# Optimization experiments

Measured on AMD Instinct MI355X. Metric: run time of the kernel, lower is better.

Reference implementation:

```python
import jax, jax.numpy as jnp
import numpy as np

N = 4096
IN_F = 256
OUT_F = 64
K = 4
ALPHA = 0.2  # LeakyReLU negative slope
NEG_INF = -9e15


def setup_inputs() -> dict:
    key = jax.random.key(0)
    k_h, k_w, k_a, k_e, k_m = jax.random.split(key, 5)
    h = jax.random.normal(k_h, (N, IN_F), dtype=jnp.float32)
    # xavier_uniform with gain=1.414
    def xavier(k, shape, gain=1.414):
        fan_in, fan_out = shape[0], shape[1]
        limit = gain * np.sqrt(6.0 / (fan_in + fan_out))
        return jax.random.uniform(k, shape, jnp.float32, -limit, limit)
    W = xavier(k_w, (IN_F, OUT_F))
    a = xavier(k_a, (2 * OUT_F, 1))
    vals = jax.random.uniform(k_e, (K, N, N), dtype=jnp.float32)
    mask = jax.random.uniform(k_m, (K, N, N), dtype=jnp.float32) < 0.05
    edge_attr = jnp.where(mask, vals, 0.0)
    return {"h": h, "edge_attr": edge_attr, "W": W, "a": a}


def reference(h, edge_attr, W, a):
    # h: [N, IN_F], edge_attr: [K, N, N], W: [IN_F, OUT_F], a: [2*OUT_F, 1]
    Wh = h @ W                                   # [N, OUT_F]
    Wh1 = Wh @ a[:OUT_F, :]                      # [N, 1]
    Wh2 = Wh @ a[OUT_F:, :]                      # [N, 1]
    e = jax.nn.leaky_relu(Wh1 + Wh2.T, negative_slope=ALPHA)  # [N, N]
    e = e[None, :, :] * edge_attr                # [K, N, N]
    e = jnp.where(edge_attr > 0, e, NEG_INF)
    att = jax.nn.softmax(e, axis=1)              # softmax over dim=1, as in torch
    # dropout is identity in eval mode
    # batched replacement for the per-channel python loop of matmuls
    hp = jnp.einsum('kij,jf->kif', att, Wh)      # [K, N, OUT_F]
    out = jnp.transpose(hp, (1, 0, 2)).reshape(N, K * OUT_F)  # concat dim=1
    return jax.nn.elu(out), att
```

## Files before the change

### kernel.cpp

```cpp
#include <hip/hip_runtime.h>

#define NN 4096
#define IN_F 256
#define OUT_F 64
#define K_CH 4
#define ALPHA 0.2f
#define ROWS1 32
#define IC1 128
#define BSTRIDE 264

typedef __bf16 bf16;
typedef __attribute__((ext_vector_type(8))) __bf16 bf16x8;
typedef __attribute__((ext_vector_type(4))) __bf16 bf16x4;
typedef __attribute__((ext_vector_type(4))) float f32x4;

__global__ __launch_bounds__(256) void k0_wh(const float* __restrict__ h,
                                             const float* __restrict__ W,
                                             const float* __restrict__ a,
                                             float* __restrict__ Wh,
                                             float* __restrict__ Wh1,
                                             float* __restrict__ Wh2) {
    int tid = threadIdx.x;
    int wave = tid >> 6, lane = tid & 63;
    int i = blockIdx.x * 4 + wave;
    const float* hrow = h + (size_t)i * IN_F;
    float acc = 0.f;
    #pragma unroll 8
    for (int c = 0; c < IN_F; ++c)
        acc += hrow[c] * W[c * OUT_F + lane];
    Wh[(size_t)i * OUT_F + lane] = acc;
    float v1 = acc * a[lane];
    float v2 = acc * a[OUT_F + lane];
    #pragma unroll
    for (int o = 32; o > 0; o >>= 1) {
        v1 += __shfl_xor(v1, o, 64);
        v2 += __shfl_xor(v2, o, 64);
    }
    if (lane == 0) { Wh1[i] = v1; Wh2[i] = v2; }
}

__global__ __launch_bounds__(256) void k0_transpose(const float* __restrict__ Wh,
                                                    bf16* __restrict__ WhT) {
    __shared__ float lds[OUT_F * 65];
    int tid = threadIdx.x;
    int i0 = blockIdx.x * 64;
    int f = tid & 63;
    int r0 = tid >> 6;
    #pragma unroll
    for (int s = 0; s < 16; ++s) {
        int r = r0 * 16 + s;
        lds[f * 65 + r] = Wh[(size_t)(i0 + r) * OUT_F + f];
    }
    __syncthreads();
    int f2 = tid >> 2;
    int c0 = (tid & 3) * 16;
    bf16x8 v0, v1;
    #pragma unroll
    for (int s = 0; s < 8; ++s) {
        v0[s] = (bf16)lds[f2 * 65 + c0 + s];
        v1[s] = (bf16)lds[f2 * 65 + c0 + 8 + s];
    }
    *(bf16x8*)&WhT[(size_t)f2 * NN + i0 + c0] = v0;
    *(bf16x8*)&WhT[(size_t)f2 * NN + i0 + c0 + 8] = v1;
}

__global__ __launch_bounds__(256) void k1_colsum(const float* __restrict__ edge,
                                                 const float* __restrict__ Wh1,
                                                 const float* __restrict__ Wh2,
                                                 bf16* __restrict__ p_buf,
                                                 float* __restrict__ partial) {
    int tid = threadIdx.x;
    int kch = blockIdx.z;
    int j0 = blockIdx.y * 1024 + tid * 4;
    int ic = blockIdx.x;
    int ibase = ic * ROWS1;
    f32x4 w2 = *(const f32x4*)&Wh2[j0];
    f32x4 w1v[ROWS1 / 4];
    #pragma unroll
    for (int t = 0; t < ROWS1 / 4; ++t)
        w1v[t] = *(const f32x4*)&Wh1[ibase + t * 4];
    f32x4 s = {0.f, 0.f, 0.f, 0.f};
    const float* base = edge + ((size_t)kch * NN + ibase) * NN + j0;
    bf16* pbase = p_buf + ((size_t)kch * NN + ibase) * NN + j0;
    f32x4 r[8];
    #pragma unroll
    for (int t = 0; t < 8; ++t)
        r[t] = __builtin_nontemporal_load((const f32x4*)(base + (size_t)t * NN));
    #pragma unroll
    for (int ii = 0; ii < ROWS1; ++ii) {
        int cur = ii & 7;
        f32x4 e = r[cur];
        int ip = (ii + 8 < ROWS1) ? ii + 8 : ii;
        r[cur] = __builtin_nontemporal_load((const f32x4*)(base + (size_t)ip * NN));
        float wh1 = w1v[ii >> 2][ii & 3];
        bf16x4 pv;
        #pragma unroll
        for (int c = 0; c < 4; ++c) {
            float xv = wh1 + w2[c];
            float lk = xv > 0.f ? xv : ALPHA * xv;
            float val = e[c] > 0.f ? __expf(lk * e[c]) : 0.f;
            bf16 vb = (bf16)val;
            pv[c] = vb;
            s[c] += (float)vb;
        }
        *(bf16x4*)(pbase + (size_t)ii * NN) = pv;
    }
    *(f32x4*)(partial + ((size_t)kch * IC1 + ic) * NN + j0) = s;
}

__global__ __launch_bounds__(256) void k1_reduce(const float* __restrict__ partial,
                                                 const bf16* __restrict__ WhT,
                                                 float* __restrict__ s_inv,
                                                 bf16* __restrict__ WhTs) {
    __shared__ float red[256];
    __shared__ float inv_l[64];
    int tid = threadIdx.x;
    int kch = blockIdx.y;
    int jl = tid & 63, g = tid >> 6;
    int jbase = blockIdx.x * 64;
    int j = jbase + jl;
    const float* pb = partial + (size_t)kch * IC1 * NN;
    float s = 0.f;
    #pragma unroll 8
    for (int t = 0; t < IC1 / 4; ++t)
        s += pb[(size_t)(g * (IC1 / 4) + t) * NN + j];
    red[tid] = s;
    __syncthreads();
    if (tid < 64) {
        float tot = red[tid] + red[tid + 64] + red[tid + 128] + red[tid + 192];
        float iv = tot > 0.f ? 1.f / tot : 0.f;
        s_inv[kch * NN + j] = iv;
        inv_l[tid] = iv;
    }
    __syncthreads();
    int f = tid >> 2;
    int c0 = (tid & 3) * 16;
    bf16x8 a0 = *(const bf16x8*)&WhT[(size_t)f * NN + jbase + c0];
    bf16x8 a1 = *(const bf16x8*)&WhT[(size_t)f * NN + jbase + c0 + 8];
    bf16x8 o0, o1;
    #pragma unroll
    for (int s2 = 0; s2 < 8; ++s2) {
        o0[s2] = (bf16)((float)a0[s2] * inv_l[c0 + s2]);
        o1[s2] = (bf16)((float)a1[s2] * inv_l[c0 + 8 + s2]);
    }
    bf16* wb = WhTs + ((size_t)kch * OUT_F + f) * NN + jbase + c0;
    *(bf16x8*)wb = o0;
    *(bf16x8*)(wb + 8) = o1;
}

__global__ __launch_bounds__(256) void k2_mfma(const bf16* __restrict__ p_buf,
                                               const bf16* __restrict__ WhTs,
                                               float* __restrict__ out) {
    __shared__ bf16 ldsB[OUT_F * BSTRIDE];
    int tid = threadIdx.x;
    int itile = blockIdx.x;
    int kch = blockIdx.y;
    int wave = tid >> 6, lane = tid & 63;
    int n16 = lane & 15, quad = lane >> 4;
    int i_row = itile * 64 + wave * 16 + n16;
    const bf16* pptr = p_buf + ((size_t)kch * NN + i_row) * NN + quad * 8;
    f32x4 acc[4] = {};
    bf16x8 pf[8];
    #pragma unroll
    for (int t = 0; t < 8; ++t)
        pf[t] = __builtin_nontemporal_load((const bf16x8*)(pptr + t * 32));
    int f = tid >> 2, part = (tid & 3) * 64;
    const bf16* wsrc = WhTs + ((size_t)kch * OUT_F + f) * NN + part;
    for (int slab = 0; slab < 16; ++slab) {
        __syncthreads();
        #pragma unroll
        for (int u = 0; u < 8; ++u) {
            bf16x8 v = *(const bf16x8*)(wsrc + slab * 256 + u * 8);
            *(bf16x8*)&ldsB[f * BSTRIDE + part + u * 8] = v;
        }
        __syncthreads();
        #pragma unroll
        for (int t = 0; t < 8; ++t) {
            int g = slab * 8 + t;
            int cur = g & 7;
            bf16x8 afrag = pf[cur];
            int gp = (g + 8 < 128) ? g + 8 : g;
            pf[cur] = __builtin_nontemporal_load((const bf16x8*)(pptr + gp * 32));
            int jl = t * 32 + quad * 8;
            #pragma unroll
            for (int ft = 0; ft < 4; ++ft) {
                bf16x8 bfrag = *(const bf16x8*)&ldsB[(ft * 16 + n16) * BSTRIDE + jl];
                acc[ft] = __builtin_amdgcn_mfma_f32_16x16x32_bf16(afrag, bfrag, acc[ft], 0, 0, 0);
            }
        }
    }
    #pragma unroll
    for (int ft = 0; ft < 4; ++ft) {
        #pragma unroll
        for (int r = 0; r < 4; ++r) {
            int row_l = quad * 4 + r;
            int i_g = itile * 64 + wave * 16 + row_l;
            float v = acc[ft][r];
            out[(size_t)i_g * (K_CH * OUT_F) + kch * OUT_F + ft * 16 + n16] =
                v > 0.f ? v : __expf(v) - 1.f;
        }
    }
}

__global__ __launch_bounds__(256) void k2_att(const bf16* __restrict__ p_buf,
                                              const float* __restrict__ s_inv,
                                              float* __restrict__ att_out) {
    int kch = blockIdx.y;
    const bf16* pb = p_buf + (size_t)kch * NN * NN;
    float* ab = att_out + (size_t)kch * NN * NN;
    const float* inv = s_inv + kch * NN;
    #pragma unroll
    for (int it = 0; it < 4; ++it) {
        size_t chunk = ((size_t)it * 2048 + blockIdx.x) * 256 + threadIdx.x;
        size_t base = chunk * 8;
        int j0 = (int)(base & (NN - 1));
        bf16x8 pv = __builtin_nontemporal_load((const bf16x8*)(pb + base));
        f32x4 iv0 = *(const f32x4*)&inv[j0];
        f32x4 iv1 = *(const f32x4*)&inv[j0 + 4];
        f32x4 a0, a1;
        #pragma unroll
        for (int c = 0; c < 4; ++c) {
            a0[c] = (float)pv[c] * iv0[c];
            a1[c] = (float)pv[c + 4] * iv1[c];
        }
        __builtin_nontemporal_store(a0, (f32x4*)(ab + base));
        __builtin_nontemporal_store(a1, (f32x4*)(ab + base + 4));
    }
}

extern "C" void kernel_launch(void* const* d_in, const int* in_sizes, int n_in,
                              void* d_out, int out_size, void* d_ws, size_t ws_size,
                              hipStream_t stream) {
    (void)out_size; (void)ws_size;
    const float *h = nullptr, *edge = nullptr, *W = nullptr, *a = nullptr;
    for (int i = 0; i < n_in; ++i) {
        int sz = in_sizes[i];
        if (sz == NN * IN_F)               h    = (const float*)d_in[i];
        else if (sz == K_CH * NN * NN)     edge = (const float*)d_in[i];
        else if (sz == IN_F * OUT_F)       W    = (const float*)d_in[i];
        else if (sz == 2 * OUT_F)          a    = (const float*)d_in[i];
    }

    char* ws = (char*)d_ws;
    size_t off = 0;
    float* Wh      = (float*)(ws + off); off += (size_t)NN * OUT_F * 4;
    float* Wh1     = (float*)(ws + off); off += NN * 4;
    float* Wh2     = (float*)(ws + off); off += NN * 4;
    float* s_inv   = (float*)(ws + off); off += (size_t)K_CH * NN * 4;
    bf16*  WhT     = (bf16*) (ws + off); off += (size_t)OUT_F * NN * 2;
    bf16*  WhTs    = (bf16*) (ws + off); off += (size_t)K_CH * OUT_F * NN * 2;
    float* partial = (float*)(ws + off); off += (size_t)K_CH * IC1 * NN * 4;
    bf16*  p_buf   = (bf16*) (ws + off); off += (size_t)K_CH * NN * NN * 2;

    float* out_h   = (float*)d_out;
    float* att_out = out_h + (size_t)NN * (K_CH * OUT_F);

    k0_wh<<<dim3(NN / 4), 256, 0, stream>>>(h, W, a, Wh, Wh1, Wh2);
    k0_transpose<<<dim3(NN / 64), 256, 0, stream>>>(Wh, WhT);
    k1_colsum<<<dim3(IC1, 4, K_CH), 256, 0, stream>>>(edge, Wh1, Wh2, p_buf, partial);
    k1_reduce<<<dim3(NN / 64, K_CH), 256, 0, stream>>>(partial, WhT, s_inv, WhTs);
    k2_mfma<<<dim3(64, K_CH), 256, 0, stream>>>(p_buf, WhTs, out_h);
    k2_att<<<dim3(2048, K_CH), 256, 0, stream>>>(p_buf, s_inv, att_out);
}
```

Before: 565.2 us.

## Recompute attention weights from edge data instead of materializing bf16 buffer

Drops the bf16 p_buf intermediate. The column-sum kernel now only produces partial sums. A fused kernel re-reads edge_attr, recomputes the exponentials, writes the normalized attention, and feeds the MFMA aggregation in one pass. The j dimension is split into four chunks for more blocks, with a small ELU reduction kernel summing the partial outputs. This removes a write and two reads of the large bf16 buffer in exchange for a second read of the fp32 edge tensor and extra exp work.

```diff
diff --git a/kernel.cpp b/kernel.cpp
--- a/kernel.cpp
+++ b/kernel.cpp
@@ -67,7 +67,6 @@
 __global__ __launch_bounds__(256) void k1_colsum(const float* __restrict__ edge,
                                                  const float* __restrict__ Wh1,
                                                  const float* __restrict__ Wh2,
-                                                 bf16* __restrict__ p_buf,
                                                  float* __restrict__ partial) {
     int tid = threadIdx.x;
     int kch = blockIdx.z;
@@ -81,29 +80,24 @@
         w1v[t] = *(const f32x4*)&Wh1[ibase + t * 4];
     f32x4 s = {0.f, 0.f, 0.f, 0.f};
     const float* base = edge + ((size_t)kch * NN + ibase) * NN + j0;
-    bf16* pbase = p_buf + ((size_t)kch * NN + ibase) * NN + j0;
     f32x4 r[8];
     #pragma unroll
     for (int t = 0; t < 8; ++t)
-        r[t] = __builtin_nontemporal_load((const f32x4*)(base + (size_t)t * NN));
+        r[t] = *(const f32x4*)(base + (size_t)t * NN);
     #pragma unroll
     for (int ii = 0; ii < ROWS1; ++ii) {
-        int cur = ii & 7;
-        f32x4 e = r[cur];
-        int ip = (ii + 8 < ROWS1) ? ii + 8 : ii;
-        r[cur] = __builtin_nontemporal_load((const f32x4*)(base + (size_t)ip * NN));
+        f32x4 e = r[ii & 7];
+        if (ii + 8 < ROWS1)
+            r[ii & 7] = *(const f32x4*)(base + (size_t)(ii + 8) * NN);
         float wh1 = w1v[ii >> 2][ii & 3];
-        bf16x4 pv;
         #pragma unroll
         for (int c = 0; c < 4; ++c) {
             float xv = wh1 + w2[c];
             float lk = xv > 0.f ? xv : ALPHA * xv;
             float val = e[c] > 0.f ? __expf(lk * e[c]) : 0.f;
             bf16 vb = (bf16)val;
-            pv[c] = vb;
             s[c] += (float)vb;
         }
-        *(bf16x4*)(pbase + (size_t)ii * NN) = pv;
     }
     *(f32x4*)(partial + ((size_t)kch * IC1 + ic) * NN + j0) = s;
 }
@@ -148,25 +142,38 @@
     *(bf16x8*)(wb + 8) = o1;
 }
 
-__global__ __launch_bounds__(256) void k2_mfma(const bf16* __restrict__ p_buf,
-                                               const bf16* __restrict__ WhTs,
-                                               float* __restrict__ out) {
+__global__ __launch_bounds__(256, 4) void k2_fused(const float* __restrict__ edge,
+                                                   const float* __restrict__ Wh1,
+                                                   const float* __restrict__ Wh2,
+                                                   const float* __restrict__ s_inv,
+                                                   const bf16* __restrict__ WhTs,
+                                                   float* __restrict__ att_out,
+                                                   float* __restrict__ hp_part) {
     __shared__ bf16 ldsB[OUT_F * BSTRIDE];
     int tid = threadIdx.x;
     int itile = blockIdx.x;
-    int kch = blockIdx.y;
+    int jq = blockIdx.y;
+    int kch = blockIdx.z;
     int wave = tid >> 6, lane = tid & 63;
     int n16 = lane & 15, quad = lane >> 4;
     int i_row = itile * 64 + wave * 16 + n16;
-    const bf16* pptr = p_buf + ((size_t)kch * NN + i_row) * NN + quad * 8;
+    int jbase = jq * 1024;
+    const float* erow = edge + ((size_t)kch * NN + i_row) * NN + jbase + quad * 8;
+    float* arow = att_out + ((size_t)kch * NN + i_row) * NN + jbase + quad * 8;
+    const float* w2p = Wh2 + jbase + quad * 8;
+    const float* ivp = s_inv + kch * NN + jbase + quad * 8;
+    float wh1 = Wh1[i_row];
     f32x4 acc[4] = {};
-    bf16x8 pf[8];
-    #pragma unroll
-    for (int t = 0; t < 8; ++t)
-        pf[t] = __builtin_nontemporal_load((const bf16x8*)(pptr + t * 32));
+    f32x4 pf0[4], pf1[4];
+    #pragma unroll
+    for (int t = 0; t < 4; ++t) {
+        pf0[t] = *(const f32x4*)(erow + t * 32);
+        pf1[t] = *(const f32x4*)(erow + t * 32 + 4);
+    }
     int f = tid >> 2, part = (tid & 3) * 64;
-    const bf16* wsrc = WhTs + ((size_t)kch * OUT_F + f) * NN + part;
-    for (int slab = 0; slab < 16; ++slab) {
+    const bf16* wsrc = WhTs + ((size_t)kch * OUT_F + f) * NN + jbase + part;
+    #pragma unroll
+    for (int slab = 0; slab < 4; ++slab) {
         __syncthreads();
         #pragma unroll
         for (int u = 0; u < 8; ++u) {
@@ -177,10 +184,33 @@
         #pragma unroll
         for (int t = 0; t < 8; ++t) {
             int g = slab * 8 + t;
-            int cur = g & 7;
-            bf16x8 afrag = pf[cur];
-            int gp = (g + 8 < 128) ? g + 8 : g;
-            pf[cur] = __builtin_nontemporal_load((const bf16x8*)(pptr + gp * 32));
+            int cur = g & 3;
+            f32x4 e0 = pf0[cur], e1 = pf1[cur];
+            if (g + 4 < 32) {
+                pf0[cur] = *(const f32x4*)(erow + (g + 4) * 32);
+                pf1[cur] = *(const f32x4*)(erow + (g + 4) * 32 + 4);
+            }
+            f32x4 w2a = *(const f32x4*)(w2p + g * 32);
+            f32x4 w2b = *(const f32x4*)(w2p + g * 32 + 4);
+            f32x4 iva = *(const f32x4*)(ivp + g * 32);
+            f32x4 ivb = *(const f32x4*)(ivp + g * 32 + 4);
+            bf16x8 afrag;
+            f32x4 av0, av1;
+            #pragma unroll
+            for (int c = 0; c < 8; ++c) {
+                float e  = c < 4 ? e0[c]  : e1[c - 4];
+                float wv = c < 4 ? w2a[c] : w2b[c - 4];
+                float iv = c < 4 ? iva[c] : ivb[c - 4];
+                float xv = wh1 + wv;
+                float lk = xv > 0.f ? xv : ALPHA * xv;
+                float val = e > 0.f ? __expf(lk * e) : 0.f;
+                bf16 vb = (bf16)val;
+                afrag[c] = vb;
+                float attv = (float)vb * iv;
+                if (c < 4) av0[c] = attv; else av1[c - 4] = attv;
+            }
+            *(f32x4*)(arow + g * 32) = av0;
+            *(f32x4*)(arow + g * 32 + 4) = av1;
             int jl = t * 32 + quad * 8;
             #pragma unroll
             for (int ft = 0; ft < 4; ++ft) {
@@ -189,43 +219,27 @@
             }
         }
     }
+    float* hb = hp_part + (((size_t)kch * 4 + jq) * NN) * OUT_F;
     #pragma unroll
     for (int ft = 0; ft < 4; ++ft) {
         #pragma unroll
         for (int r = 0; r < 4; ++r) {
-            int row_l = quad * 4 + r;
-            int i_g = itile * 64 + wave * 16 + row_l;
-            float v = acc[ft][r];
-            out[(size_t)i_g * (K_CH * OUT_F) + kch * OUT_F + ft * 16 + n16] =
-                v > 0.f ? v : __expf(v) - 1.f;
-        }
-    }
-}
-
-__global__ __launch_bounds__(256) void k2_att(const bf16* __restrict__ p_buf,
-                                              const float* __restrict__ s_inv,
-                                              float* __restrict__ att_out) {
-    int kch = blockIdx.y;
-    const bf16* pb = p_buf + (size_t)kch * NN * NN;
-    float* ab = att_out + (size_t)kch * NN * NN;
-    const float* inv = s_inv + kch * NN;
-    #pragma unroll
-    for (int it = 0; it < 4; ++it) {
-        size_t chunk = ((size_t)it * 2048 + blockIdx.x) * 256 + threadIdx.x;
-        size_t base = chunk * 8;
-        int j0 = (int)(base & (NN - 1));
-        bf16x8 pv = __builtin_nontemporal_load((const bf16x8*)(pb + base));
-        f32x4 iv0 = *(const f32x4*)&inv[j0];
-        f32x4 iv1 = *(const f32x4*)&inv[j0 + 4];
-        f32x4 a0, a1;
-        #pragma unroll
-        for (int c = 0; c < 4; ++c) {
-            a0[c] = (float)pv[c] * iv0[c];
-            a1[c] = (float)pv[c + 4] * iv1[c];
-        }
-        __builtin_nontemporal_store(a0, (f32x4*)(ab + base));
-        __builtin_nontemporal_store(a1, (f32x4*)(ab + base + 4));
-    }
+            int i_g = itile * 64 + wave * 16 + quad * 4 + r;
+            hb[(size_t)i_g * OUT_F + ft * 16 + n16] = acc[ft][r];
+        }
+    }
+}
+
+__global__ __launch_bounds__(256) void k3_elu(const float* __restrict__ hp_part,
+                                              float* __restrict__ out) {
+    int i = blockIdx.x;
+    int tid = threadIdx.x;
+    int kch = tid >> 6, f = tid & 63;
+    float s = 0.f;
+    #pragma unroll
+    for (int jq = 0; jq < 4; ++jq)
+        s += hp_part[(((size_t)kch * 4 + jq) * NN + i) * OUT_F + f];
+    out[(size_t)i * (K_CH * OUT_F) + tid] = s > 0.f ? s : __expf(s) - 1.f;
 }
 
 extern "C" void kernel_launch(void* const* d_in, const int* in_sizes, int n_in,
@@ -250,15 +264,16 @@
     bf16*  WhT     = (bf16*) (ws + off); off += (size_t)OUT_F * NN * 2;
     bf16*  WhTs    = (bf16*) (ws + off); off += (size_t)K_CH * OUT_F * NN * 2;
     float* partial = (float*)(ws + off); off += (size_t)K_CH * IC1 * NN * 4;
-    bf16*  p_buf   = (bf16*) (ws + off); off += (size_t)K_CH * NN * NN * 2;
+    float* hp_part = (float*)(ws + off); off += (size_t)K_CH * 4 * NN * OUT_F * 4;
 
     float* out_h   = (float*)d_out;
     float* att_out = out_h + (size_t)NN * (K_CH * OUT_F);
 
     k0_wh<<<dim3(NN / 4), 256, 0, stream>>>(h, W, a, Wh, Wh1, Wh2);
     k0_transpose<<<dim3(NN / 64), 256, 0, stream>>>(Wh, WhT);
-    k1_colsum<<<dim3(IC1, 4, K_CH), 256, 0, stream>>>(edge, Wh1, Wh2, p_buf, partial);
+    k1_colsum<<<dim3(IC1, 4, K_CH), 256, 0, stream>>>(edge, Wh1, Wh2, partial);
     k1_reduce<<<dim3(NN / 64, K_CH), 256, 0, stream>>>(partial, WhT, s_inv, WhTs);
-    k2_mfma<<<dim3(64, K_CH), 256, 0, stream>>>(p_buf, WhTs, out_h);
-    k2_att<<<dim3(2048, K_CH), 256, 0, stream>>>(p_buf, s_inv, att_out);
-}
+    k2_fused<<<dim3(64, 4, K_CH), 256, 0, stream>>>(edge, Wh1, Wh2, s_inv, WhTs,
+                                                    att_out, hp_part);
+    k3_elu<<<dim3(NN), 256, 0, stream>>>(hp_part, out_h);
+}
```

New measurement: 579.8 us. 2.6% more time.
